# Kernel tuning notes

Hardware: AMD Instinct MI355X
Metric: run time of the kernel (lower is better)

Reference implementation:

```python
import jax, jax.numpy as jnp
import numpy as np
from math import sqrt

T, B, V = 32, 16, 30000
D, DQKV = 300, 150
K, G = 10, 32            # top-K globals, grapharea_size neighbours each
S = 25000                # last_idx_senses (= SC rows)
EPS = 1e-8


def setup_inputs() -> dict:
    key = jax.random.key(0)
    ks = jax.random.split(key, 6)
    return {
        "predictions_globals": jax.random.normal(ks[0], (T, B, V), jnp.float32),
        "location_context": jax.random.normal(ks[1], (T, B, D), jnp.float32),
        "SC": jax.random.normal(ks[2], (S, D), jnp.float32),
        "Wq": jax.random.normal(ks[3], (D, DQKV), jnp.float32) / sqrt(D),
        "Wk": jax.random.normal(ks[4], (D, DQKV), jnp.float32) / sqrt(D),
        "neighbours_table": jax.random.randint(ks[5], (V, G), 0, S, jnp.int64),
    }


def reference(predictions_globals, location_context, SC, Wq, Wk, neighbours_table):
    # 1) per-sample top-K global selection (sort descending, take K indices)
    _, topk_idx = jax.lax.top_k(predictions_globals, K)          # [T,B,K]
    # 2) sense-neighbour lookup: K globals x G neighbours -> N = K*G senses
    neigh = neighbours_table[topk_idx].reshape(T, B, K * G)      # [T,B,N] int
    # 3) gather precomputed sense contexts
    senses_context = SC[neigh]                                   # [T,B,N,D]
    # 4) ComputeLogits: QK attention logits
    q = location_context @ Wq                                    # [T,B,dqkv]
    k = senses_context @ Wk                                      # [T,B,N,dqkv]
    logits = jnp.einsum("tbd,tbnd->tbn", q, k) / sqrt(DQKV)      # [T,B,N]
    # 5) softmax over neighbours, scatter into full sense distribution
    p = jax.nn.softmax(logits, axis=-1)                          # [T,B,N]
    base = jnp.full((T * B, S), EPS, dtype=p.dtype)
    rows = jnp.arange(T * B)[:, None]                            # [TB,1]
    senses_softmax = base.at[rows, neigh.reshape(T * B, -1)].set(p.reshape(T * B, -1))
    # 6) log-probabilities over all senses
    return jnp.log(senses_softmax)                               # [T*B, S]
```

## Files before the change

kernel.cpp:

```cpp
#include <hip/hip_runtime.h>
#include <math.h>

#define T_ 32
#define B_ 16
#define V_ 30000
#define V4 7500
#define D_ 300
#define DQKV_ 150
#define K_ 10
#define G_ 32
#define N_ 320
#define S_ 25000
#define S4 6250
#define NTS 1024
#define NTA 512
#define LCAP 4096
#define UTH 0xC0000000u

__device__ __forceinline__ unsigned umap(float f) {
    unsigned b = __float_as_uint(f);
    unsigned mask = (unsigned)(((int)b) >> 31);
    return b ^ (mask | 0x80000000u);
}
__device__ __forceinline__ bool better_u(unsigned au, int ai, unsigned bu, int bi) {
    return (au > bu) || (au == bu && ai < bi);
}

__global__ __launch_bounds__(NTS, 2) void scan_kernel(
    const float* __restrict__ pred, float* __restrict__ out,
    int* __restrict__ wstop)
{
    const int row = blockIdx.x, tid = threadIdx.x;
    const int lane = tid & 63, wave = tid >> 6;
    __shared__ unsigned lu[LCAP];
    __shared__ int      li[LCAP];
    __shared__ int      cnt;

    if (tid == 0) cnt = 0;
    __syncthreads();

    const float FILL = -18.420680743952367f;
    {
        float4 f4 = make_float4(FILL, FILL, FILL, FILL);
        float4* o4 = (float4*)(out + (size_t)row * S_);
        #pragma unroll
        for (int k = 0; k < 7; ++k) { int i = tid + k * NTS; if (i < S4) o4[i] = f4; }
    }

    {
        const float4* p4 = (const float4*)(pred + (size_t)row * V_);
        #pragma unroll
        for (int k = 0; k < 8; ++k) {
            int i = tid + k * NTS;
            if (i < V4) {
                float4 v = p4[i];
                unsigned u0 = umap(v.x), u1 = umap(v.y), u2 = umap(v.z), u3 = umap(v.w);
                int base = i * 4;
                if (u0 >= UTH) { int p = atomicAdd(&cnt, 1); if (p < LCAP) { lu[p] = u0; li[p] = base; } }
                if (u1 >= UTH) { int p = atomicAdd(&cnt, 1); if (p < LCAP) { lu[p] = u1; li[p] = base + 1; } }
                if (u2 >= UTH) { int p = atomicAdd(&cnt, 1); if (p < LCAP) { lu[p] = u2; li[p] = base + 2; } }
                if (u3 >= UTH) { int p = atomicAdd(&cnt, 1); if (p < LCAP) { lu[p] = u3; li[p] = base + 3; } }
            }
        }
    }
    __syncthreads();
    const int c = cnt;

    if (c >= K_ && c <= LCAP) {
        if (wave == 0) {
            for (int p = 0; p < K_; ++p) {
                unsigned bu = 0; int bi = 0x7fffffff;
                for (int s = lane; s < c; s += 64) {
                    unsigned uu = lu[s]; int ii = li[s];
                    if (better_u(uu, ii, bu, bi)) { bu = uu; bi = ii; }
                }
                #pragma unroll
                for (int off = 32; off; off >>= 1) {
                    unsigned ou = __shfl_xor(bu, off, 64);
                    int      oi = __shfl_xor(bi, off, 64);
                    if (better_u(ou, oi, bu, bi)) { bu = ou; bi = oi; }
                }
                if (lane == 0) wstop[row * K_ + p] = bi;
                for (int s = lane; s < c; s += 64)
                    if (li[s] == bi && lu[s] == bu) lu[s] = 0;
            }
        }
    } else {
        if (wave == 0) {
            unsigned tu[K_]; int tix[K_];
            #pragma unroll
            for (int s = 0; s < K_; ++s) { tu[s] = 0; tix[s] = 0x7fffffff; }
            const float* prow = pred + (size_t)row * V_;
            for (int i = lane; i < V_; i += 64) {
                unsigned u = umap(prow[i]);
                if (better_u(u, i, tu[K_-1], tix[K_-1])) {
                    tu[K_-1] = u; tix[K_-1] = i;
                    #pragma unroll
                    for (int s = K_-1; s > 0; --s)
                        if (better_u(tu[s], tix[s], tu[s-1], tix[s-1])) {
                            unsigned a = tu[s]; tu[s] = tu[s-1]; tu[s-1] = a;
                            int b2 = tix[s]; tix[s] = tix[s-1]; tix[s-1] = b2;
                        }
                }
            }
            for (int p = 0; p < K_; ++p) {
                unsigned bu = tu[0]; int bi = tix[0];
                #pragma unroll
                for (int s = 1; s < K_; ++s)
                    if (better_u(tu[s], tix[s], bu, bi)) { bu = tu[s]; bi = tix[s]; }
                #pragma unroll
                for (int off = 32; off; off >>= 1) {
                    unsigned ou = __shfl_xor(bu, off, 64);
                    int      oi = __shfl_xor(bi, off, 64);
                    if (better_u(ou, oi, bu, bi)) { bu = ou; bi = oi; }
                }
                if (lane == 0) wstop[row * K_ + p] = bi;
                #pragma unroll
                for (int s = 0; s < K_; ++s)
                    if (tix[s] == bi) tu[s] = 0;
            }
        }
    }
}

__global__ __launch_bounds__(NTA) void attn_kernel(
    const float* __restrict__ lc, const float* __restrict__ SC,
    const float* __restrict__ Wq, const float* __restrict__ Wk,
    const int* __restrict__ nbt, const int* __restrict__ wstop,
    float* __restrict__ out)
{
    const int row = blockIdx.x, tid = threadIdx.x;
    const int lane = tid & 63, wave = tid >> 6;
    __shared__ int   topg[K_];
    __shared__ __align__(16) float lcs[D_];
    __shared__ float qpart[2][DQKV_];
    __shared__ __align__(16) float qks[D_];
    __shared__ int   nidx[N_];
    __shared__ float lg[N_];
    __shared__ int   kills[N_];
    __shared__ float redA[8], redB[8];
    float* outrow = out + (size_t)row * S_;

    if (tid < K_) topg[tid] = wstop[row * K_ + tid];
    if (tid >= 64 && tid < 64 + D_ / 4)
        ((float4*)lcs)[tid - 64] = ((const float4*)(lc + (size_t)row * D_))[tid - 64];
    for (int i = tid; i < N_; i += NTA) kills[i] = 0;
    __syncthreads();

    if (tid < N_) nidx[tid] = nbt[topg[tid >> 5] * G_ + (tid & 31)];
    if (tid < 2 * DQKV_) {
        int h = tid / DQKV_;
        int j = tid - h * DQKV_;
        int d0 = h * 150;
        const float* wp = Wq + (size_t)d0 * DQKV_ + j;
        float acc = 0.f;
        #pragma unroll 10
        for (int dd = 0; dd < 150; ++dd)
            acc += lcs[d0 + dd] * wp[(size_t)dd * DQKV_];
        qpart[h][j] = acc;
    }
    __syncthreads();

    {
        float qv0 = qpart[0][lane] + qpart[1][lane];
        float qv1 = qpart[0][64 + lane] + qpart[1][64 + lane];
        float qv2 = (lane < 22) ? (qpart[0][128 + lane] + qpart[1][128 + lane]) : 0.f;
        #pragma unroll 2
        for (int d = wave; d < D_; d += 8) {
            const float* wr = Wk + (size_t)d * DQKV_;
            float w0 = wr[lane];
            float w1 = wr[64 + lane];
            float w2 = (lane < 22) ? wr[128 + lane] : 0.f;
            float p = w0 * qv0 + w1 * qv1 + w2 * qv2;
            #pragma unroll
            for (int off = 32; off; off >>= 1) p += __shfl_xor(p, off, 64);
            if (lane == 0) qks[d] = p;
        }
    }
    __syncthreads();

    const float ISC = 0.08164965809277260327f;
    const float4* q4 = (const float4*)qks;
    for (int s = tid; s < 8 * N_; s += NTA) {
        int n = s >> 3, h = s & 7;
        const float4* sc4 = (const float4*)(SC + (size_t)nidx[n] * D_);
        int c0 = h * 9;
        float acc = 0.f;
        #pragma unroll
        for (int cc = 0; cc < 9; ++cc) {
            float4 a = sc4[c0 + cc];
            float4 b = q4[c0 + cc];
            acc += a.x * b.x + a.y * b.y + a.z * b.z + a.w * b.w;
        }
        if (h < 3) {
            float4 a = sc4[72 + h];
            float4 b = q4[72 + h];
            acc += a.x * b.x + a.y * b.y + a.z * b.z + a.w * b.w;
        }
        acc += __shfl_xor(acc, 1, 64);
        acc += __shfl_xor(acc, 2, 64);
        acc += __shfl_xor(acc, 4, 64);
        if (h == 0) lg[n] = acc * ISC;
    }
    __syncthreads();

    float v = (tid < N_) ? lg[tid] : -INFINITY;
    float m = v;
    #pragma unroll
    for (int off = 32; off; off >>= 1) m = fmaxf(m, __shfl_xor(m, off, 64));
    if (lane == 0) redA[wave] = m;
    __syncthreads();
    m = redA[0];
    #pragma unroll
    for (int w = 1; w < 8; ++w) m = fmaxf(m, redA[w]);

    float ss = (tid < N_) ? expf(v - m) : 0.f;
    #pragma unroll
    for (int off = 32; off; off >>= 1) ss += __shfl_xor(ss, off, 64);
    if (lane == 0) redB[wave] = ss;
    __syncthreads();
    float tot = redB[0];
    #pragma unroll
    for (int w = 1; w < 8; ++w) tot += redB[w];
    float lsum = logf(tot);

    for (int s = tid; s < 4 * N_; s += NTA) {
        int n = s >> 2, cix = s & 3;
        int sidx = nidx[n];
        int clo = cix * 80;
        int lo = (n + 1 > clo) ? n + 1 : clo;
        int hi = clo + 80;
        bool mt = false;
        #pragma unroll 4
        for (int n2 = lo; n2 < hi; ++n2) mt |= (nidx[n2] == sidx);
        if (mt) kills[n] = 1;
    }
    __syncthreads();

    if (tid < N_ && !kills[tid]) outrow[nidx[tid]] = (v - m) - lsum;
}

#define NWS 16
__device__ __forceinline__ bool better(float av, int ai, float bv, int bi) {
    return (av > bv) || (av == bv && ai < bi);
}
__global__ __launch_bounds__(NTS, 4) void selfatt_fused(
    const float* __restrict__ pred, const float* __restrict__ lc,
    const float* __restrict__ SC, const float* __restrict__ Wq,
    const float* __restrict__ Wk, const int* __restrict__ nbt,
    float* __restrict__ out)
{
    const int row = blockIdx.x, tid = threadIdx.x;
    const int lane = tid & 63, wave = tid >> 6;
    __shared__ float wcv[NWS * K_];
    __shared__ int   wci[NWS * K_];
    __shared__ int   topg[K_];
    __shared__ float lcs[D_];
    __shared__ float qs[DQKV_];
    __shared__ __align__(16) float qks[D_];
    __shared__ int   nidx[N_];
    __shared__ float lg[N_];
    __shared__ int   kills[N_];
    __shared__ float redA[NWS], redB[NWS];
    float* outrow = out + (size_t)row * S_;
    const float FILL = -18.420680743952367f;
    {
        float4 f4 = make_float4(FILL, FILL, FILL, FILL);
        float4* o4 = (float4*)outrow;
        #pragma unroll
        for (int k = 0; k < 7; ++k) { int i = tid + k * NTS; if (i < S4) o4[i] = f4; }
    }
    float tv[K_]; int ti[K_];
    #pragma unroll
    for (int s = 0; s < K_; ++s) { tv[s] = -INFINITY; ti[s] = 0x7fffffff; }
    {
        const float4* p4 = (const float4*)(pred + (size_t)row * V_);
        const float4 NEG = make_float4(-INFINITY, -INFINITY, -INFINITY, -INFINITY);
        float4 a[8]; int ib[8];
        #pragma unroll
        for (int u = 0; u < 8; ++u) {
            int i = tid + u * NTS;
            a[u]  = (i < V4) ? p4[i] : NEG;
            ib[u] = (i < V4) ? i * 4 : 0x7ffffff0;
        }
        #pragma unroll
        for (int u = 0; u < 8; ++u) {
            float x = a[u].x, y = a[u].y, z = a[u].z, w = a[u].w;
            float m4 = fmaxf(fmaxf(x, y), fmaxf(z, w));
            if (!(m4 < tv[K_-1])) {
                float vals[4] = {x, y, z, w};
                #pragma unroll
                for (int cc = 0; cc < 4; ++cc) {
                    float val = vals[cc];
                    int   idx = ib[u] + cc;
                    if (better(val, idx, tv[K_-1], ti[K_-1])) {
                        tv[K_-1] = val; ti[K_-1] = idx;
                        #pragma unroll
                        for (int s = K_-1; s > 0; --s) {
                            if (better(tv[s], ti[s], tv[s-1], ti[s-1])) {
                                float fx = tv[s]; tv[s] = tv[s-1]; tv[s-1] = fx;
                                int   iy = ti[s]; ti[s] = ti[s-1]; ti[s-1] = iy;
                            }
                        }
                    }
                }
            }
        }
    }
    for (int p = 0; p < K_; ++p) {
        float bv = tv[0]; int bi = ti[0];
        #pragma unroll
        for (int s = 1; s < K_; ++s)
            if (better(tv[s], ti[s], bv, bi)) { bv = tv[s]; bi = ti[s]; }
        #pragma unroll
        for (int off = 32; off; off >>= 1) {
            float ov = __shfl_xor(bv, off, 64);
            int   oi = __shfl_xor(bi, off, 64);
            if (better(ov, oi, bv, bi)) { bv = ov; bi = oi; }
        }
        if (lane == 0) { wcv[wave * K_ + p] = bv; wci[wave * K_ + p] = bi; }
        #pragma unroll
        for (int s = 0; s < K_; ++s)
            if (ti[s] == bi) tv[s] = -INFINITY;
    }
    __syncthreads();
    if (wave == 0) {
        float c0v = wcv[lane],      c1v = wcv[64 + lane];
        int   c0i = wci[lane],      c1i = wci[64 + lane];
        float c2v = (lane < 32) ? wcv[128 + lane] : -INFINITY;
        int   c2i = (lane < 32) ? wci[128 + lane] : 0x7fffffff;
        for (int p = 0; p < K_; ++p) {
            float bv = c0v; int bi = c0i;
            if (better(c1v, c1i, bv, bi)) { bv = c1v; bi = c1i; }
            if (better(c2v, c2i, bv, bi)) { bv = c2v; bi = c2i; }
            #pragma unroll
            for (int off = 32; off; off >>= 1) {
                float ov = __shfl_xor(bv, off, 64);
                int   oi = __shfl_xor(bi, off, 64);
                if (better(ov, oi, bv, bi)) { bv = ov; bi = oi; }
            }
            if (lane == 0) topg[p] = bi;
            if (c0i == bi) c0v = -INFINITY;
            if (c1i == bi) c1v = -INFINITY;
            if (c2i == bi) c2v = -INFINITY;
        }
    }
    __syncthreads();
    if (tid < N_) { int g = topg[tid >> 5]; nidx[tid] = nbt[g * G_ + (tid & 31)]; }
    else if (tid < 2 * N_) kills[tid - N_] = 0;
    else if (tid >= 640 && tid < 640 + D_) lcs[tid - 640] = lc[(size_t)row * D_ + (tid - 640)];
    __syncthreads();
    if (tid < 600) {
        int j = tid >> 2, h = tid & 3;
        int d0 = h * 75;
        const float* wp = Wq + (size_t)d0 * DQKV_ + j;
        float acc = 0.f;
        #pragma unroll 5
        for (int dd = 0; dd < 75; ++dd) acc += lcs[d0 + dd] * wp[(size_t)dd * DQKV_];
        acc += __shfl_xor(acc, 1, 64);
        acc += __shfl_xor(acc, 2, 64);
        if (h == 0) qs[j] = acc;
    } else {
        int t0 = tid - 600;
        for (int s = t0; s < 4 * N_; s += 424) {
            int n = s >> 2, cc = s & 3;
            int sidx = nidx[n];
            int clo = cc * 80;
            int lo = (n + 1 > clo) ? n + 1 : clo;
            int hi = clo + 80;
            bool mt = false;
            #pragma unroll 4
            for (int n2 = lo; n2 < hi; ++n2) mt |= (nidx[n2] == sidx);
            if (mt) kills[n] = 1;
        }
    }
    __syncthreads();
    if (tid < 600) {
        int d = tid >> 1, h = tid & 1;
        int j0 = h * 75;
        const float* wrow = Wk + (size_t)d * DQKV_ + j0;
        float acc = 0.f;
        #pragma unroll 5
        for (int jj = 0; jj < 75; ++jj) acc += wrow[jj] * qs[j0 + jj];
        acc += __shfl_xor(acc, 1, 64);
        if (h == 0) qks[d] = acc;
    }
    __syncthreads();
    const float ISC = 0.08164965809277260327f;
    const float4* q4 = (const float4*)qks;
    for (int s = tid; s < 8 * N_; s += NTS) {
        int n = s >> 3, h = s & 7;
        const float4* sc4 = (const float4*)(SC + (size_t)nidx[n] * D_);
        int c0 = h * 9;
        float acc = 0.f;
        #pragma unroll
        for (int cc = 0; cc < 9; ++cc) {
            float4 a = sc4[c0 + cc];
            float4 b = q4[c0 + cc];
            acc += a.x * b.x + a.y * b.y + a.z * b.z + a.w * b.w;
        }
        if (h < 3) {
            float4 a = sc4[72 + h];
            float4 b = q4[72 + h];
            acc += a.x * b.x + a.y * b.y + a.z * b.z + a.w * b.w;
        }
        acc += __shfl_xor(acc, 1, 64);
        acc += __shfl_xor(acc, 2, 64);
        acc += __shfl_xor(acc, 4, 64);
        if (h == 0) lg[n] = acc * ISC;
    }
    __syncthreads();
    float v = (tid < N_) ? lg[tid] : -INFINITY;
    float m = v;
    #pragma unroll
    for (int off = 32; off; off >>= 1) m = fmaxf(m, __shfl_xor(m, off, 64));
    if (lane == 0) redA[wave] = m;
    __syncthreads();
    m = redA[0];
    #pragma unroll
    for (int w = 1; w < NWS; ++w) m = fmaxf(m, redA[w]);
    float e = (tid < N_) ? expf(v - m) : 0.f;
    float ss = e;
    #pragma unroll
    for (int off = 32; off; off >>= 1) ss += __shfl_xor(ss, off, 64);
    if (lane == 0) redB[wave] = ss;
    __syncthreads();
    float tot = redB[0];
    #pragma unroll
    for (int w = 1; w < NWS; ++w) tot += redB[w];
    float lsum = logf(tot);
    if (tid < N_ && !kills[tid]) outrow[nidx[tid]] = (v - m) - lsum;
}

extern "C" void kernel_launch(void* const* d_in, const int* in_sizes, int n_in,
                              void* d_out, int out_size, void* d_ws, size_t ws_size,
                              hipStream_t stream) {
    const float* pred = (const float*)d_in[0];
    const float* lc   = (const float*)d_in[1];
    const float* SC   = (const float*)d_in[2];
    const float* Wq   = (const float*)d_in[3];
    const float* Wk   = (const float*)d_in[4];
    const int*   nbt  = (const int*)d_in[5];
    float* out = (float*)d_out;

    const size_t need = (size_t)T_ * B_ * K_ * sizeof(int);
    if (ws_size >= need) {
        int* wstop = (int*)d_ws;
        scan_kernel<<<dim3(T_ * B_), dim3(NTS), 0, stream>>>(pred, out, wstop);
        attn_kernel<<<dim3(T_ * B_), dim3(NTA), 0, stream>>>(
            lc, SC, Wq, Wk, nbt, wstop, out);
    } else {
        selfatt_fused<<<dim3(T_ * B_), dim3(NTS), 0, stream>>>(
            pred, lc, SC, Wq, Wk, nbt, out);
    }
}
```

Before: 103.5 us.

## Split attention into scan+prep, SC-slice-partitioned gather, and finalize kernels

Moves the neighbour lookup and q·Wk projection into the top-K scan kernel and writes them to workspace. The SC gather then becomes a separate kernel with 8 blocks per row, each handling only the neighbours whose sense index falls in its slice of SC, so concurrently running blocks touch smaller SC regions and may get better L2 locality. A third kernel does the softmax, duplicate removal and scatter. This adds two kernel launches and a round-trip through global workspace, and the workspace requirement grows, which could push execution onto the fused fallback path.

```diff
diff --git a/kernel.cpp b/kernel.cpp
--- a/kernel.cpp
+++ b/kernel.cpp
@@ -12,8 +12,11 @@
 #define N_ 320
 #define S_ 25000
 #define S4 6250
+#define SLICE 3125
+#define QKP 304
 #define NTS 1024
-#define NTA 512
+#define NTG 256
+#define NTF 384
 #define LCAP 4096
 #define UTH 0xC0000000u
 
@@ -26,15 +29,20 @@
     return (au > bu) || (au == bu && ai < bi);
 }
 
-__global__ __launch_bounds__(NTS, 2) void scan_kernel(
-    const float* __restrict__ pred, float* __restrict__ out,
-    int* __restrict__ wstop)
+__global__ __launch_bounds__(NTS, 2) void scan_prep_kernel(
+    const float* __restrict__ pred, const float* __restrict__ lc,
+    const float* __restrict__ Wq, const float* __restrict__ Wk,
+    const int* __restrict__ nbt,
+    float* __restrict__ out, float* __restrict__ qkws, int* __restrict__ nidxws)
 {
     const int row = blockIdx.x, tid = threadIdx.x;
     const int lane = tid & 63, wave = tid >> 6;
     __shared__ unsigned lu[LCAP];
     __shared__ int      li[LCAP];
     __shared__ int      cnt;
+    __shared__ int      topg[K_];
+    __shared__ __align__(16) float lcs[D_];
+    __shared__ float    qpart[4][DQKV_];
 
     if (tid == 0) cnt = 0;
     __syncthreads();
@@ -80,7 +88,7 @@
                     int      oi = __shfl_xor(bi, off, 64);
                     if (better_u(ou, oi, bu, bi)) { bu = ou; bi = oi; }
                 }
-                if (lane == 0) wstop[row * K_ + p] = bi;
+                if (lane == 0) topg[p] = bi;
                 for (int s = lane; s < c; s += 64)
                     if (li[s] == bi && lu[s] == bu) lu[s] = 0;
             }
@@ -114,59 +122,39 @@
                     int      oi = __shfl_xor(bi, off, 64);
                     if (better_u(ou, oi, bu, bi)) { bu = ou; bi = oi; }
                 }
-                if (lane == 0) wstop[row * K_ + p] = bi;
+                if (lane == 0) topg[p] = bi;
                 #pragma unroll
                 for (int s = 0; s < K_; ++s)
                     if (tix[s] == bi) tu[s] = 0;
             }
         }
     }
-}
-
-__global__ __launch_bounds__(NTA) void attn_kernel(
-    const float* __restrict__ lc, const float* __restrict__ SC,
-    const float* __restrict__ Wq, const float* __restrict__ Wk,
-    const int* __restrict__ nbt, const int* __restrict__ wstop,
-    float* __restrict__ out)
-{
-    const int row = blockIdx.x, tid = threadIdx.x;
-    const int lane = tid & 63, wave = tid >> 6;
-    __shared__ int   topg[K_];
-    __shared__ __align__(16) float lcs[D_];
-    __shared__ float qpart[2][DQKV_];
-    __shared__ __align__(16) float qks[D_];
-    __shared__ int   nidx[N_];
-    __shared__ float lg[N_];
-    __shared__ int   kills[N_];
-    __shared__ float redA[8], redB[8];
-    float* outrow = out + (size_t)row * S_;
-
-    if (tid < K_) topg[tid] = wstop[row * K_ + tid];
-    if (tid >= 64 && tid < 64 + D_ / 4)
-        ((float4*)lcs)[tid - 64] = ((const float4*)(lc + (size_t)row * D_))[tid - 64];
-    for (int i = tid; i < N_; i += NTA) kills[i] = 0;
-    __syncthreads();
-
-    if (tid < N_) nidx[tid] = nbt[topg[tid >> 5] * G_ + (tid & 31)];
-    if (tid < 2 * DQKV_) {
+    __syncthreads();
+
+    if (tid < N_) nidxws[(size_t)row * N_ + tid] = nbt[topg[tid >> 5] * G_ + (tid & 31)];
+    if (tid >= 384 && tid < 384 + D_ / 4)
+        ((float4*)lcs)[tid - 384] = ((const float4*)(lc + (size_t)row * D_))[tid - 384];
+    __syncthreads();
+
+    if (tid < 4 * DQKV_) {
         int h = tid / DQKV_;
         int j = tid - h * DQKV_;
-        int d0 = h * 150;
+        int d0 = h * 75;
         const float* wp = Wq + (size_t)d0 * DQKV_ + j;
         float acc = 0.f;
-        #pragma unroll 10
-        for (int dd = 0; dd < 150; ++dd)
+        #pragma unroll 5
+        for (int dd = 0; dd < 75; ++dd)
             acc += lcs[d0 + dd] * wp[(size_t)dd * DQKV_];
         qpart[h][j] = acc;
     }
     __syncthreads();
 
     {
-        float qv0 = qpart[0][lane] + qpart[1][lane];
-        float qv1 = qpart[0][64 + lane] + qpart[1][64 + lane];
-        float qv2 = (lane < 22) ? (qpart[0][128 + lane] + qpart[1][128 + lane]) : 0.f;
-        #pragma unroll 2
-        for (int d = wave; d < D_; d += 8) {
+        float qv0 = qpart[0][lane] + qpart[1][lane] + qpart[2][lane] + qpart[3][lane];
+        float qv1 = qpart[0][64 + lane] + qpart[1][64 + lane] + qpart[2][64 + lane] + qpart[3][64 + lane];
+        float qv2 = (lane < 22) ? (qpart[0][128 + lane] + qpart[1][128 + lane]
+                                 + qpart[2][128 + lane] + qpart[3][128 + lane]) : 0.f;
+        for (int d = wave; d < D_; d += 16) {
             const float* wr = Wk + (size_t)d * DQKV_;
             float w0 = wr[lane];
             float w1 = wr[64 + lane];
@@ -174,16 +162,44 @@
             float p = w0 * qv0 + w1 * qv1 + w2 * qv2;
             #pragma unroll
             for (int off = 32; off; off >>= 1) p += __shfl_xor(p, off, 64);
-            if (lane == 0) qks[d] = p;
-        }
-    }
-    __syncthreads();
+            if (lane == 0) qkws[(size_t)row * QKP + d] = p;
+        }
+    }
+}
+
+__global__ __launch_bounds__(NTG) void gather_kernel(
+    const float* __restrict__ SC, const float* __restrict__ qkws,
+    const int* __restrict__ nidxws, float* __restrict__ logws)
+{
+    const int r = blockIdx.x >> 3;
+    const int ch = blockIdx.x & 7;
+    const int lo = ch * SLICE, hi = lo + SLICE;
+    const int tid = threadIdx.x;
+    __shared__ int   nid[N_];
+    __shared__ __align__(16) float qk[D_];
+    __shared__ int   list[N_];
+    __shared__ int   lcnt;
+
+    if (tid == 0) lcnt = 0;
+    for (int i = tid; i < N_; i += NTG)
+        nid[i] = nidxws[(size_t)r * N_ + i];
+    if (tid < D_ / 4)
+        ((float4*)qk)[tid] = ((const float4*)(qkws + (size_t)r * QKP))[tid];
+    __syncthreads();
+
+    for (int i = tid; i < N_; i += NTG) {
+        int sv = nid[i];
+        if (sv >= lo && sv < hi) { int p = atomicAdd(&lcnt, 1); list[p] = i; }
+    }
+    __syncthreads();
+    const int c2 = lcnt;
 
     const float ISC = 0.08164965809277260327f;
-    const float4* q4 = (const float4*)qks;
-    for (int s = tid; s < 8 * N_; s += NTA) {
-        int n = s >> 3, h = s & 7;
-        const float4* sc4 = (const float4*)(SC + (size_t)nidx[n] * D_);
+    const float4* q4 = (const float4*)qk;
+    for (int s = tid; s < 8 * c2; s += NTG) {
+        int g = s >> 3, h = s & 7;
+        int n = list[g];
+        const float4* sc4 = (const float4*)(SC + (size_t)nid[n] * D_);
         int c0 = h * 9;
         float acc = 0.f;
         #pragma unroll
@@ -200,7 +216,26 @@
         acc += __shfl_xor(acc, 1, 64);
         acc += __shfl_xor(acc, 2, 64);
         acc += __shfl_xor(acc, 4, 64);
-        if (h == 0) lg[n] = acc * ISC;
+        if (h == 0) logws[(size_t)r * N_ + n] = acc * ISC;
+    }
+}
+
+__global__ __launch_bounds__(NTF) void finalize_kernel(
+    const float* __restrict__ logws, const int* __restrict__ nidxws,
+    float* __restrict__ out)
+{
+    const int row = blockIdx.x, tid = threadIdx.x;
+    const int lane = tid & 63, wave = tid >> 6;
+    __shared__ float lg[N_];
+    __shared__ int   nid[N_];
+    __shared__ int   kills[N_];
+    __shared__ float redA[6], redB[6];
+    float* outrow = out + (size_t)row * S_;
+
+    if (tid < N_) {
+        lg[tid]  = logws[(size_t)row * N_ + tid];
+        nid[tid] = nidxws[(size_t)row * N_ + tid];
+        kills[tid] = 0;
     }
     __syncthreads();
 
@@ -212,7 +247,7 @@
     __syncthreads();
     m = redA[0];
     #pragma unroll
-    for (int w = 1; w < 8; ++w) m = fmaxf(m, redA[w]);
+    for (int w = 1; w < 6; ++w) m = fmaxf(m, redA[w]);
 
     float ss = (tid < N_) ? expf(v - m) : 0.f;
     #pragma unroll
@@ -221,23 +256,23 @@
     __syncthreads();
     float tot = redB[0];
     #pragma unroll
-    for (int w = 1; w < 8; ++w) tot += redB[w];
+    for (int w = 1; w < 6; ++w) tot += redB[w];
     float lsum = logf(tot);
 
-    for (int s = tid; s < 4 * N_; s += NTA) {
+    for (int s = tid; s < 4 * N_; s += NTF) {
         int n = s >> 2, cix = s & 3;
-        int sidx = nidx[n];
+        int sidx = nid[n];
         int clo = cix * 80;
-        int lo = (n + 1 > clo) ? n + 1 : clo;
-        int hi = clo + 80;
+        int lo2 = (n + 1 > clo) ? n + 1 : clo;
+        int hi2 = clo + 80;
         bool mt = false;
         #pragma unroll 4
-        for (int n2 = lo; n2 < hi; ++n2) mt |= (nidx[n2] == sidx);
+        for (int n2 = lo2; n2 < hi2; ++n2) mt |= (nid[n2] == sidx);
         if (mt) kills[n] = 1;
     }
     __syncthreads();
 
-    if (tid < N_ && !kills[tid]) outrow[nidx[tid]] = (v - m) - lsum;
+    if (tid < N_ && !kills[tid]) outrow[nid[tid]] = (v - m) - lsum;
 }
 
 #define NWS 16
@@ -443,12 +478,22 @@
     const int*   nbt  = (const int*)d_in[5];
     float* out = (float*)d_out;
 
-    const size_t need = (size_t)T_ * B_ * K_ * sizeof(int);
+    const int nrows = T_ * B_;
+    const size_t nQK = (size_t)nrows * QKP;
+    const size_t nNI = (size_t)nrows * N_;
+    const size_t nLG = (size_t)nrows * N_;
+    const size_t need = (nQK + nLG) * sizeof(float) + nNI * sizeof(int);
+
     if (ws_size >= need) {
-        int* wstop = (int*)d_ws;
-        scan_kernel<<<dim3(T_ * B_), dim3(NTS), 0, stream>>>(pred, out, wstop);
-        attn_kernel<<<dim3(T_ * B_), dim3(NTA), 0, stream>>>(
-            lc, SC, Wq, Wk, nbt, wstop, out);
+        float* qkws   = (float*)d_ws;
+        int*   nidxws = (int*)(qkws + nQK);
+        float* logws  = (float*)(nidxws + nNI);
+        scan_prep_kernel<<<dim3(nrows), dim3(NTS), 0, stream>>>(
+            pred, lc, Wq, Wk, nbt, out, qkws, nidxws);
+        gather_kernel<<<dim3(nrows * 8), dim3(NTG), 0, stream>>>(
+            SC, qkws, nidxws, logws);
+        finalize_kernel<<<dim3(nrows), dim3(NTF), 0, stream>>>(
+            logws, nidxws, out);
     } else {
         selfatt_fused<<<dim3(T_ * B_), dim3(NTS), 0, stream>>>(
             pred, lc, SC, Wq, Wk, nbt, out);
```

New measurement: 126.5 us. 22.3% more time.
